# Performance work log

Hardware: AMD Instinct MI355X
Metric: run time of the kernel (lower is better)

Reference implementation:

```python
import jax, jax.numpy as jnp
import numpy as np

N_NODES = 50000
N_EDGES = 800000
NFEAT, NHID, NCLASS, NCLUSTER = 512, 64, 16, 32


def gcn_conv(x, W, b, edge_index, edge_weight, n):
    """PyG GCNConv: add self-loops, symmetric normalization, linear + scatter-add."""
    row, col = edge_index[0], edge_index[1]
    loop = jnp.arange(n, dtype=row.dtype)
    row = jnp.concatenate([row, loop])
    col = jnp.concatenate([col, loop])
    w = jnp.concatenate([edge_weight, jnp.ones((n,), dtype=edge_weight.dtype)])
    # degree computed on target index (gcn_norm convention)
    deg = jax.ops.segment_sum(w, col, num_segments=n)
    dinv = jnp.where(deg > 0, jax.lax.rsqrt(deg), 0.0)
    norm = dinv[row] * w * dinv[col]          # [E+n]
    xw = x @ W                                # [n, out]
    msg = xw[row] * norm[:, None]             # gather + scale
    out = jax.ops.segment_sum(msg, col, num_segments=n)  # scatter-add
    return out + b


def setup_inputs() -> dict:
    key = jax.random.key(0)
    ks = jax.random.split(key, 12)
    def glorot(k, fan_in, fan_out):
        s = np.sqrt(6.0 / (fan_in + fan_out)).astype(np.float32)
        return jax.random.uniform(k, (fan_in, fan_out), jnp.float32, -s, s)
    x = jax.random.normal(ks[0], (N_NODES, NFEAT), jnp.float32)
    edge_index = jax.random.randint(ks[1], (2, N_EDGES), 0, N_NODES, dtype=jnp.int64)
    edge_weight = jax.random.uniform(ks[2], (N_EDGES,), jnp.float32)
    return {
        "x": x, "edge_index": edge_index, "edge_weight": edge_weight,
        "W1": glorot(ks[3], NFEAT, NHID), "b1": jnp.zeros((NHID,), jnp.float32),
        "W2": glorot(ks[4], NHID, NHID), "b2": jnp.zeros((NHID,), jnp.float32),
        "fcW1": glorot(ks[5], NHID, NCLASS), "fcb1": jnp.zeros((NCLASS,), jnp.float32),
        "fcW2": glorot(ks[6], NHID, NCLUSTER), "fcb2": jnp.zeros((NCLUSTER,), jnp.float32),
    }


def reference(x, edge_index, edge_weight, W1, b1, W2, b2, fcW1, fcb1, fcW2, fcb2):
    n = x.shape[0]
    h = jax.nn.relu(gcn_conv(x, W1, b1, edge_index, edge_weight, n))
    # dropout omitted (eval-mode / deterministic reference)
    h = gcn_conv(h, W2, b2, edge_index, edge_weight, n)
    pred = h @ fcW1 + fcb1
    pred_cluster = h @ fcW2 + fcb2
    return (pred, pred_cluster)
```

## Files before the change

### kernel.cpp

```cpp
#include <hip/hip_runtime.h>
#include <hip/hip_bf16.h>
#include <cstdint>
#include <cstddef>

#define N_FEAT 512
#define N_HID 64
#define N_CLASS 16
#define N_CLUSTER 32
#define NPART 8

typedef short short8 __attribute__((ext_vector_type(8)));
typedef float floatx4 __attribute__((ext_vector_type(4)));
typedef unsigned short u16;
typedef unsigned short u16x4 __attribute__((ext_vector_type(4)));
typedef unsigned short u16x8 __attribute__((ext_vector_type(8)));

__device__ __forceinline__ short f2bf(float f) {
  __hip_bfloat16 h = __float2bfloat16(f);
  return *reinterpret_cast<short*>(&h);
}
__device__ __forceinline__ u16 f2bfu(float f) { return (u16)f2bf(f); }
__device__ __forceinline__ float bf2f(u16 u) {
  return __uint_as_float((unsigned)u << 16);
}

__device__ __forceinline__ void prepBF_one(const float* __restrict__ W,
                                           short* __restrict__ BF, int K, int idx) {
  int lane = idx & 63;
  int sj = idx >> 6;
  int j = sj & 3, s = sj >> 2;
  int col = j * 16 + (lane & 15);
  int k0 = s * 32 + ((lane >> 4) << 3);
  short8 v;
  #pragma unroll
  for (int t = 0; t < 8; ++t) v[t] = f2bf(W[(size_t)(k0 + t) * 64 + col]);
  *(short8*)(BF + (size_t)idx * 8) = v;
}

__global__ void k_init(uint4* __restrict__ h16, int n16,
                       const float* __restrict__ W1, short* __restrict__ BF1,
                       const float* __restrict__ W2, short* __restrict__ BF2,
                       int nbZ) {
  int b = blockIdx.x, t = threadIdx.x;
  if (b < nbZ) {
    int i = b * 256 + t;
    if (i < n16) h16[i] = make_uint4(0u, 0u, 0u, 0u);
  } else if (b < nbZ + 16) {
    prepBF_one(W1, BF1, N_FEAT, (b - nbZ) * 256 + t);
  } else {
    int idx = (b - nbZ - 16) * 256 + t;
    if (idx < 512) prepBF_one(W2, BF2, N_HID, idx);
  }
}

__global__ __launch_bounds__(256, 4) void k_fusedA(
    const float* __restrict__ x, u16* __restrict__ xbf, int nf8,
    const int* __restrict__ coli, const float* __restrict__ w,
    unsigned long long* __restrict__ hist, int* __restrict__ rank,
    int H, int E, int nbE) {
  const int q = blockIdx.x / 5;
  const int r = blockIdx.x % 5;
  if (r == 0) {
    if (q >= nbE) return;
    int e = q * 256 + threadIdx.x;
    if (e >= E) return;
    int p = q & (NPART - 1);
    int c = coli[e];
    unsigned long long fx = (unsigned long long)__float2uint_rn(w[e] * 16777216.0f);
    unsigned long long old = atomicAdd(&hist[(size_t)p * H + c], (1ull << 40) | fx);
    rank[e] = (int)(old >> 40);
  } else {
    int i = (q * 4 + (r - 1)) * 256 + threadIdx.x;
    if (i >= nf8) return;
    float4 a0 = *(const float4*)(x + (size_t)i * 8);
    float4 a1 = *(const float4*)(x + (size_t)i * 8 + 4);
    u16x8 o;
    o[0] = f2bfu(a0.x); o[1] = f2bfu(a0.y); o[2] = f2bfu(a0.z); o[3] = f2bfu(a0.w);
    o[4] = f2bfu(a1.x); o[5] = f2bfu(a1.y); o[6] = f2bfu(a1.z); o[7] = f2bfu(a1.w);
    *(u16x8*)(xbf + (size_t)i * 8) = o;
  }
}

__global__ __launch_bounds__(256) void k_redscan(
    const unsigned long long* __restrict__ hist, int H,
    float* __restrict__ dinv, int* __restrict__ off,
    int* __restrict__ bsum, int n) {
  __shared__ int sh[256];
  int t = threadIdx.x;
  int i = blockIdx.x * 256 + t;
  int v = 0;
  if (i < n) {
    unsigned long long tot = 0;
    #pragma unroll
    for (int p = 0; p < NPART; ++p) tot += hist[(size_t)p * H + i];
    v = (int)(tot >> 40);
    float wsum = (float)(tot & ((1ull << 40) - 1)) * 5.9604644775390625e-08f;
    dinv[i] = rsqrtf(1.0f + wsum);
  }
  sh[t] = v;
  __syncthreads();
  #pragma unroll
  for (int d = 1; d < 256; d <<= 1) {
    int x = 0;
    if (t >= d) x = sh[t - d];
    __syncthreads();
    if (t >= d) sh[t] += x;
    __syncthreads();
  }
  if (i < n) off[i] = sh[t] - v;
  if (t == 255) bsum[blockIdx.x] = sh[255];
}

__global__ __launch_bounds__(256) void k_scan2(const int* __restrict__ bsum,
                                               int* __restrict__ bsum2, int nb) {
  __shared__ int sh[256];
  int t = threadIdx.x;
  int v = (t < nb) ? bsum[t] : 0;
  sh[t] = v;
  __syncthreads();
  #pragma unroll
  for (int d = 1; d < 256; d <<= 1) {
    int x = 0;
    if (t >= d) x = sh[t - d];
    __syncthreads();
    if (t >= d) sh[t] += x;
    __syncthreads();
  }
  if (t < nb) bsum2[t] = sh[t] - v;
}

__global__ void k_scan3_initcur(int* __restrict__ off, const int* __restrict__ bsum2,
                                const unsigned long long* __restrict__ hist, int H,
                                int* __restrict__ cur, int n, int E) {
  int i = blockIdx.x * 256 + threadIdx.x;
  if (i < n) {
    int o = off[i] + bsum2[blockIdx.x];
    off[i] = o;
    int running = o;
    #pragma unroll
    for (int p = 0; p < NPART; ++p) {
      cur[(size_t)p * H + i] = running;
      running += (int)(hist[(size_t)p * H + i] >> 40);
    }
  }
  if (i == 0) off[n] = E;
}

__device__ __forceinline__ void gemm_wave_bf(
    const u16* __restrict__ A, const short8* __restrict__ BF,
    u16* __restrict__ C, int M, int tile) {
  const int lane = threadIdx.x & 63;
  const int rbase = tile * 16;
  int r = rbase + (lane & 15);
  if (r >= M) r = M - 1;
  const u16* arow = A + (size_t)r * 512 + ((lane >> 4) << 3);
  const short8* bbase = BF + lane;

  short8 pa[4];
  short8 pb[2][4];
  #pragma unroll
  for (int s = 0; s < 4; ++s)
    pa[s] = *(const short8*)(arow + s * 32);
  #pragma unroll
  for (int s = 0; s < 2; ++s)
    #pragma unroll
    for (int j = 0; j < 4; ++j)
      pb[s][j] = bbase[(s * 4 + j) * 64];
  __builtin_amdgcn_sched_barrier(0);

  floatx4 acc[4];
  #pragma unroll
  for (int j = 0; j < 4; ++j) acc[j] = (floatx4){0.f, 0.f, 0.f, 0.f};

  #pragma unroll
  for (int s = 0; s < 16; ++s) {
    const int sa = s & 3;
    const int sb = s & 1;
    short8 af = pa[sa];
    acc[0] = __builtin_amdgcn_mfma_f32_16x16x32_bf16(af, pb[sb][0], acc[0], 0, 0, 0);
    acc[1] = __builtin_amdgcn_mfma_f32_16x16x32_bf16(af, pb[sb][1], acc[1], 0, 0, 0);
    acc[2] = __builtin_amdgcn_mfma_f32_16x16x32_bf16(af, pb[sb][2], acc[2], 0, 0, 0);
    acc[3] = __builtin_amdgcn_mfma_f32_16x16x32_bf16(af, pb[sb][3], acc[3], 0, 0, 0);
    if (s + 4 < 16)
      pa[sa] = *(const short8*)(arow + (s + 4) * 32);
    if (s + 2 < 16) {
      #pragma unroll
      for (int j = 0; j < 4; ++j)
        pb[sb][j] = bbase[((s + 2) * 4 + j) * 64];
    }
    __builtin_amdgcn_sched_barrier(0);
  }

  const int srow = rbase + (lane >> 4) * 4;
  const int scol = lane & 15;
  #pragma unroll
  for (int i = 0; i < 4; ++i) {
    int rr = srow + i;
    if (rr < M) {
      #pragma unroll
      for (int j = 0; j < 4; ++j)
        C[(size_t)rr * 64 + j * 16 + scol] = f2bfu(acc[j][i]);
    }
  }
}

__global__ __launch_bounds__(256, 4) void k_fusedB(
    const u16* __restrict__ Abf, const short8* __restrict__ BF,
    u16* __restrict__ C, int M, int nbT, int S,
    const int* __restrict__ rowi, const int* __restrict__ coli,
    const float* __restrict__ w,
    const int* __restrict__ rank, const float* __restrict__ dinv,
    const int* __restrict__ cur, unsigned* __restrict__ pairs,
    int H, int E) {
  const int q = blockIdx.x / (S + 1);
  const int r = blockIdx.x % (S + 1);
  if (r == 0) {
    int tile = q * 4 + (threadIdx.x >> 6);
    if (tile < nbT) gemm_wave_bf(Abf, BF, C, M, tile);
  } else {
    int f = q * S + (r - 1);
    int e = f * 256 + threadIdx.x;
    if (e >= E) return;
    int p = f & (NPART - 1);
    int c = coli[e];
    int rr = rowi[e];
    int pos = cur[(size_t)p * H + c] + rank[e];
    pairs[pos] = ((unsigned)rr << 16) | (u16)f2bf(dinv[rr] * w[e] * dinv[c]);
  }
}

__global__ __launch_bounds__(64, 4) void k_mfma64(
    const u16* __restrict__ Av, const short8* __restrict__ BF,
    u16* __restrict__ C, int M) {
  const int lane = threadIdx.x & 63;
  const int rbase = blockIdx.x * 16;
  int r = rbase + (lane & 15);
  if (r >= M) r = M - 1;
  const int klo = (lane >> 4) * 8;
  const u16* arow = Av + (size_t)r * 64 + klo;
  const short8* bbase = BF + lane;

  short8 pah[2];
  short8 pb[2][4];
  pah[0] = *(const short8*)(arow);
  pah[1] = *(const short8*)(arow + 32);
  #pragma unroll
  for (int s = 0; s < 2; ++s)
    #pragma unroll
    for (int j = 0; j < 4; ++j)
      pb[s][j] = bbase[(s * 4 + j) * 64];

  floatx4 acc[4];
  #pragma unroll
  for (int j = 0; j < 4; ++j) acc[j] = (floatx4){0.f, 0.f, 0.f, 0.f};

  #pragma unroll
  for (int s = 0; s < 2; ++s) {
    acc[0] = __builtin_amdgcn_mfma_f32_16x16x32_bf16(pah[s], pb[s][0], acc[0], 0, 0, 0);
    acc[1] = __builtin_amdgcn_mfma_f32_16x16x32_bf16(pah[s], pb[s][1], acc[1], 0, 0, 0);
    acc[2] = __builtin_amdgcn_mfma_f32_16x16x32_bf16(pah[s], pb[s][2], acc[2], 0, 0, 0);
    acc[3] = __builtin_amdgcn_mfma_f32_16x16x32_bf16(pah[s], pb[s][3], acc[3], 0, 0, 0);
  }

  const int srow = rbase + (lane >> 4) * 4;
  const int scol = lane & 15;
  #pragma unroll
  for (int i = 0; i < 4; ++i) {
    int rr = srow + i;
    if (rr < M) {
      #pragma unroll
      for (int j = 0; j < 4; ++j)
        C[(size_t)rr * 64 + j * 16 + scol] = f2bfu(acc[j][i]);
    }
  }
}

template<bool RELU>
__global__ __launch_bounds__(256) void k_gather(
    const int* __restrict__ off, const unsigned* __restrict__ pairs,
    const float* __restrict__ dinv,
    const u16* __restrict__ xw, const float* __restrict__ bias,
    u16* __restrict__ h, int n) {
  int gid = blockIdx.x * 256 + threadIdx.x;
  int c = gid >> 6, lane = gid & 63;
  if (c >= n) return;
  float s = dinv[c]; s *= s;
  float acc = fmaf(bf2f(xw[(size_t)c * 64 + lane]), s, bias[lane]);
  int i = off[c], end = off[c + 1];
  for (; i + 7 < end; i += 8) {
    unsigned p[8];
    float v[8];
    #pragma unroll
    for (int t = 0; t < 8; ++t) p[t] = pairs[i + t];
    #pragma unroll
    for (int t = 0; t < 8; ++t)
      v[t] = bf2f(xw[(size_t)(p[t] >> 16) * 64 + lane]);
    #pragma unroll
    for (int t = 0; t < 8; ++t)
      acc = fmaf(v[t], __uint_as_float((p[t] & 0xffffu) << 16), acc);
  }
  for (; i + 1 < end; i += 2) {
    unsigned p0 = pairs[i], p1 = pairs[i + 1];
    float v0 = bf2f(xw[(size_t)(p0 >> 16) * 64 + lane]);
    float v1 = bf2f(xw[(size_t)(p1 >> 16) * 64 + lane]);
    acc = fmaf(v0, __uint_as_float((p0 & 0xffffu) << 16), acc);
    acc = fmaf(v1, __uint_as_float((p1 & 0xffffu) << 16), acc);
  }
  if (i < end) {
    unsigned p = pairs[i];
    acc = fmaf(bf2f(xw[(size_t)(p >> 16) * 64 + lane]),
               __uint_as_float((p & 0xffffu) << 16), acc);
  }
  if (RELU) acc = fmaxf(acc, 0.f);
  h[(size_t)c * 64 + lane] = f2bfu(acc);
}

__global__ __launch_bounds__(256) void k_fc(
    const u16* __restrict__ h,
    const float* __restrict__ fW1, const float* __restrict__ fb1,
    const float* __restrict__ fW2, const float* __restrict__ fb2,
    float* __restrict__ out, int M) {
  __shared__ float Hs[64][68];
  __shared__ float Ws[64][48];
  __shared__ float bs[48];
  const int t = threadIdx.x;
  const int row0 = blockIdx.x * 64;
  #pragma unroll
  for (int i = 0; i < 4; ++i) {
    int f = t + i * 256;
    int r = f >> 4, k4 = f & 15;
    int rr = row0 + r;
    float4 v = make_float4(0.f, 0.f, 0.f, 0.f);
    if (rr < M) {
      u16x4 u = *(const u16x4*)&h[(size_t)rr * 64 + k4 * 4];
      v = make_float4(bf2f(u[0]), bf2f(u[1]), bf2f(u[2]), bf2f(u[3]));
    }
    *(float4*)&Hs[r][k4 * 4] = v;
  }
  for (int f = t; f < 64 * 48; f += 256) {
    int k = f / 48, c = f - k * 48;
    Ws[k][c] = (c < 16) ? fW1[k * 16 + c] : fW2[k * 32 + (c - 16)];
  }
  if (t < 48) bs[t] = (t < 16) ? fb1[t] : fb2[t - 16];
  __syncthreads();
  const int tr = t >> 4, tc = t & 15;
  float acc[4][3] = {{0.f}};
  #pragma unroll 8
  for (int k = 0; k < 64; ++k) {
    float a[4], b[3];
    #pragma unroll
    for (int i = 0; i < 4; ++i) a[i] = Hs[tr * 4 + i][k];
    #pragma unroll
    for (int j = 0; j < 3; ++j) b[j] = Ws[k][tc * 3 + j];
    #pragma unroll
    for (int i = 0; i < 4; ++i)
      #pragma unroll
      for (int j = 0; j < 3; ++j) acc[i][j] = fmaf(a[i], b[j], acc[i][j]);
  }
  #pragma unroll
  for (int i = 0; i < 4; ++i) {
    int rr = row0 + tr * 4 + i;
    if (rr >= M) continue;
    #pragma unroll
    for (int j = 0; j < 3; ++j) {
      int c = tc * 3 + j;
      float v = acc[i][j] + bs[c];
      if (c < 16) out[(size_t)rr * 16 + c] = v;
      else out[(size_t)M * 16 + (size_t)rr * 32 + (c - 16)] = v;
    }
  }
}

extern "C" void kernel_launch(void* const* d_in, const int* in_sizes, int n_in,
                              void* d_out, int out_size, void* d_ws, size_t ws_size,
                              hipStream_t stream) {
  const float* x    = (const float*)d_in[0];
  const int*   ei   = (const int*)d_in[1];
  const float* ew   = (const float*)d_in[2];
  const float* W1   = (const float*)d_in[3];
  const float* b1   = (const float*)d_in[4];
  const float* W2   = (const float*)d_in[5];
  const float* b2   = (const float*)d_in[6];
  const float* fW1  = (const float*)d_in[7];
  const float* fb1  = (const float*)d_in[8];
  const float* fW2  = (const float*)d_in[9];
  const float* fb2  = (const float*)d_in[10];
  float* out = (float*)d_out;

  const int N = in_sizes[0] / N_FEAT;
  const int E = in_sizes[2];
  const int H = (N + 63) & ~63;
  const int* row = ei;
  const int* col = ei + E;

  char* ws = (char*)d_ws;
  float*              dinv = (float*)(ws + 0x000000);
  int*                off  = (int*)  (ws + 0x080000);
  int*                bsum = (int*)  (ws + 0x0C0000);
  int*                bsum2= (int*)  (ws + 0x0C1000);
  short*              BF1  = (short*)(ws + 0x0C8000);
  short*              BF2  = (short*)(ws + 0x0DA000);
  unsigned long long* hist = (unsigned long long*)(ws + 0x100000);
  int*                cur  = (int*)  (ws + 0x500000);
  unsigned*           pairs= (unsigned*)(ws + 0x6C0000);
  int*                rank = (int*)  (ws + 0xA00000);
  u16*                bufA = (u16*)  (ws + 0xD40000);
  u16*                bufB = (u16*)  (ws + 0x1980000);
  u16*                xbf  = (u16*)  (ws + 0x2400000);

  const int nbN  = (N + 255) / 256;
  const int nbE  = (E + 255) / 256;
  const int nbT  = (N + 15) / 16;
  const int nbG  = (N + 63) / 64;
  const int nbW  = (N * 64 + 255) / 256;
  const int nH16 = NPART * H / 2;
  const int nbZ  = (nH16 + 255) / 256;
  const int nf8  = N * N_FEAT / 8;
  const int ncv  = (nf8 + 255) / 256;

  const int QA = (nbE > (ncv + 3) / 4) ? nbE : (ncv + 3) / 4;
  const int GB = (nbT + 3) / 4;
  const int SB = (nbE + GB - 1) / GB;

  k_init<<<nbZ + 18, 256, 0, stream>>>((uint4*)hist, nH16, W1, BF1, W2, BF2, nbZ);

  k_fusedA<<<QA * 5, 256, 0, stream>>>(x, xbf, nf8, col, ew, hist, rank, H, E, nbE);

  k_redscan<<<nbN, 256, 0, stream>>>(hist, H, dinv, off, bsum, N);
  k_scan2  <<<1,   256, 0, stream>>>(bsum, bsum2, nbN);
  k_scan3_initcur<<<nbN, 256, 0, stream>>>(off, bsum2, hist, H, cur, N, E);

  k_fusedB<<<GB * (SB + 1), 256, 0, stream>>>(
      xbf, (const short8*)BF1, bufA, N, nbT, SB,
      row, col, ew, rank, dinv, cur, pairs, H, E);

  k_gather<true><<<nbW, 256, 0, stream>>>(off, pairs, dinv, bufA, b1, bufB, N);

  k_mfma64<<<nbT, 64, 0, stream>>>(bufB, (const short8*)BF2, bufA, N);
  k_gather<false><<<nbW, 256, 0, stream>>>(off, pairs, dinv, bufA, b2, bufB, N);

  k_fc<<<nbG, 256, 0, stream>>>(bufB, fW1, fb1, fW2, fb2, out, N);
}
```

Measured before the change: 172.7 us.

## Pre-swizzle bf16 x into MFMA tile layout and merge block-sum scan

```diff
diff --git a/kernel.cpp b/kernel.cpp
--- a/kernel.cpp
+++ b/kernel.cpp
@@ -54,15 +54,17 @@
 }
 
 __global__ __launch_bounds__(256, 4) void k_fusedA(
-    const float* __restrict__ x, u16* __restrict__ xbf, int nf8,
+    const float* __restrict__ x, u16* __restrict__ xbf, int M,
     const int* __restrict__ coli, const float* __restrict__ w,
     unsigned long long* __restrict__ hist, int* __restrict__ rank,
-    int H, int E, int nbE) {
-  const int q = blockIdx.x / 5;
-  const int r = blockIdx.x % 5;
+    int H, int E, int nbE, int nbT) {
+  __shared__ u16 Ls[16 * 520];
+  const int q = blockIdx.x >> 1;
+  const int r = blockIdx.x & 1;
+  const int t = threadIdx.x;
   if (r == 0) {
     if (q >= nbE) return;
-    int e = q * 256 + threadIdx.x;
+    int e = q * 256 + t;
     if (e >= E) return;
     int p = q & (NPART - 1);
     int c = coli[e];
@@ -70,14 +72,28 @@
     unsigned long long old = atomicAdd(&hist[(size_t)p * H + c], (1ull << 40) | fx);
     rank[e] = (int)(old >> 40);
   } else {
-    int i = (q * 4 + (r - 1)) * 256 + threadIdx.x;
-    if (i >= nf8) return;
-    float4 a0 = *(const float4*)(x + (size_t)i * 8);
-    float4 a1 = *(const float4*)(x + (size_t)i * 8 + 4);
-    u16x8 o;
-    o[0] = f2bfu(a0.x); o[1] = f2bfu(a0.y); o[2] = f2bfu(a0.z); o[3] = f2bfu(a0.w);
-    o[4] = f2bfu(a1.x); o[5] = f2bfu(a1.y); o[6] = f2bfu(a1.z); o[7] = f2bfu(a1.w);
-    *(u16x8*)(xbf + (size_t)i * 8) = o;
+    if (q >= nbT) return;
+    const int row0 = q * 16;
+    #pragma unroll
+    for (int i = 0; i < 8; ++i) {
+      int f = i * 256 + t;
+      int row = f >> 7, c4 = f & 127;
+      int grow = row0 + row;
+      if (grow >= M) grow = M - 1;
+      float4 v = *(const float4*)(x + (size_t)grow * 512 + c4 * 4);
+      u16x4 o;
+      o[0] = f2bfu(v.x); o[1] = f2bfu(v.y); o[2] = f2bfu(v.z); o[3] = f2bfu(v.w);
+      *(u16x4*)(Ls + row * 520 + c4 * 4) = o;
+    }
+    __syncthreads();
+    #pragma unroll
+    for (int i = 0; i < 4; ++i) {
+      int g = i * 256 + t;
+      int s = g >> 6, lane = g & 63;
+      int row = lane & 15, k0 = s * 32 + ((lane >> 4) << 3);
+      u16x8 v = *(const u16x8*)(Ls + row * 520 + k0);
+      *(u16x8*)(xbf + (size_t)q * 8192 + (size_t)g * 8) = v;
+    }
   }
 }
 
@@ -111,8 +127,10 @@
   if (t == 255) bsum[blockIdx.x] = sh[255];
 }
 
-__global__ __launch_bounds__(256) void k_scan2(const int* __restrict__ bsum,
-                                               int* __restrict__ bsum2, int nb) {
+__global__ __launch_bounds__(256) void k_scan3_initcur(
+    int* __restrict__ off, const int* __restrict__ bsum,
+    const unsigned long long* __restrict__ hist, int H,
+    int* __restrict__ cur, int n, int E, int nb) {
   __shared__ int sh[256];
   int t = threadIdx.x;
   int v = (t < nb) ? bsum[t] : 0;
@@ -126,15 +144,10 @@
     if (t >= d) sh[t] += x;
     __syncthreads();
   }
-  if (t < nb) bsum2[t] = sh[t] - v;
-}
-
-__global__ void k_scan3_initcur(int* __restrict__ off, const int* __restrict__ bsum2,
-                                const unsigned long long* __restrict__ hist, int H,
-                                int* __restrict__ cur, int n, int E) {
-  int i = blockIdx.x * 256 + threadIdx.x;
+  int base = (blockIdx.x > 0) ? sh[blockIdx.x - 1] : 0;
+  int i = blockIdx.x * 256 + t;
   if (i < n) {
-    int o = off[i] + bsum2[blockIdx.x];
+    int o = off[i] + base;
     off[i] = o;
     int running = o;
     #pragma unroll
@@ -150,17 +163,14 @@
     const u16* __restrict__ A, const short8* __restrict__ BF,
     u16* __restrict__ C, int M, int tile) {
   const int lane = threadIdx.x & 63;
-  const int rbase = tile * 16;
-  int r = rbase + (lane & 15);
-  if (r >= M) r = M - 1;
-  const u16* arow = A + (size_t)r * 512 + ((lane >> 4) << 3);
+  const u16* abase = A + (size_t)tile * 8192 + lane * 8;
   const short8* bbase = BF + lane;
 
   short8 pa[4];
   short8 pb[2][4];
   #pragma unroll
   for (int s = 0; s < 4; ++s)
-    pa[s] = *(const short8*)(arow + s * 32);
+    pa[s] = *(const short8*)(abase + s * 512);
   #pragma unroll
   for (int s = 0; s < 2; ++s)
     #pragma unroll
@@ -182,7 +192,7 @@
     acc[2] = __builtin_amdgcn_mfma_f32_16x16x32_bf16(af, pb[sb][2], acc[2], 0, 0, 0);
     acc[3] = __builtin_amdgcn_mfma_f32_16x16x32_bf16(af, pb[sb][3], acc[3], 0, 0, 0);
     if (s + 4 < 16)
-      pa[sa] = *(const short8*)(arow + (s + 4) * 32);
+      pa[sa] = *(const short8*)(abase + (s + 4) * 512);
     if (s + 2 < 16) {
       #pragma unroll
       for (int j = 0; j < 4; ++j)
@@ -191,7 +201,7 @@
     __builtin_amdgcn_sched_barrier(0);
   }
 
-  const int srow = rbase + (lane >> 4) * 4;
+  const int srow = tile * 16 + (lane >> 4) * 4;
   const int scol = lane & 15;
   #pragma unroll
   for (int i = 0; i < 4; ++i) {
@@ -397,7 +407,6 @@
   float*              dinv = (float*)(ws + 0x000000);
   int*                off  = (int*)  (ws + 0x080000);
   int*                bsum = (int*)  (ws + 0x0C0000);
-  int*                bsum2= (int*)  (ws + 0x0C1000);
   short*              BF1  = (short*)(ws + 0x0C8000);
   short*              BF2  = (short*)(ws + 0x0DA000);
   unsigned long long* hist = (unsigned long long*)(ws + 0x100000);
@@ -415,20 +424,17 @@
   const int nbW  = (N * 64 + 255) / 256;
   const int nH16 = NPART * H / 2;
   const int nbZ  = (nH16 + 255) / 256;
-  const int nf8  = N * N_FEAT / 8;
-  const int ncv  = (nf8 + 255) / 256;
-
-  const int QA = (nbE > (ncv + 3) / 4) ? nbE : (ncv + 3) / 4;
+
+  const int QA = (nbE > nbT) ? nbE : nbT;
   const int GB = (nbT + 3) / 4;
   const int SB = (nbE + GB - 1) / GB;
 
   k_init<<<nbZ + 18, 256, 0, stream>>>((uint4*)hist, nH16, W1, BF1, W2, BF2, nbZ);
 
-  k_fusedA<<<QA * 5, 256, 0, stream>>>(x, xbf, nf8, col, ew, hist, rank, H, E, nbE);
+  k_fusedA<<<QA * 2, 256, 0, stream>>>(x, xbf, N, col, ew, hist, rank, H, E, nbE, nbT);
 
   k_redscan<<<nbN, 256, 0, stream>>>(hist, H, dinv, off, bsum, N);
-  k_scan2  <<<1,   256, 0, stream>>>(bsum, bsum2, nbN);
-  k_scan3_initcur<<<nbN, 256, 0, stream>>>(off, bsum2, hist, H, cur, N, E);
+  k_scan3_initcur<<<nbN, 256, 0, stream>>>(off, bsum, hist, H, cur, N, E, nbN);
 
   k_fusedB<<<GB * (SB + 1), 256, 0, stream>>>(
       xbf, (const short8*)BF1, bufA, N, nbT, SB,
```

Result: no change. 172.2 us (-0.3%).
